# Optimization experiments

Measured on AMD Instinct MI355X. Metric: run time of the kernel, lower is better.

## Reference

```python
import jax, jax.numpy as jnp
import numpy as np

B, N, T, F_IN, H, E_RAND = 4, 1024, 12, 64, 64, 32768


def _xavier_uniform(key, shape):
    fan_in, fan_out = shape[1], shape[0]
    a = np.sqrt(6.0 / (fan_in + fan_out)).astype(np.float32)
    return jax.random.uniform(key, shape, jnp.float32, -a, a)


def setup_inputs() -> dict:
    key = jax.random.key(0)
    ks = jax.random.split(key, 6)
    x = jax.random.normal(ks[0], (B, N, T, F_IN), jnp.float32)
    src = jax.random.randint(ks[1], (E_RAND,), 0, N)
    dst = jax.random.randint(ks[2], (E_RAND,), 0, N)
    loops = jnp.arange(N)  # self-loops: guarantee every softmax row is non-empty
    edge_index = jnp.stack([jnp.concatenate([src, loops]),
                            jnp.concatenate([dst, loops])]).astype(jnp.int64)
    W = _xavier_uniform(ks[3], (H, F_IN))        # nn.Linear weight layout [out, in]
    a_l = _xavier_uniform(ks[4], (H, 1))
    a_r = _xavier_uniform(ks[5], (H, 1))
    bias = jnp.zeros((H,), jnp.float32)
    return {"x": x, "edge_index": edge_index, "W": W, "a_l": a_l, "a_r": a_r, "bias": bias}


def reference(x, edge_index, W, a_l, a_r, bias):
    n = x.shape[1]
    x_in = x.transpose(0, 2, 1, 3)                       # [B,T,N,F_in]
    h = jnp.einsum('btnf,hf->btnh', x_in, W)             # [B,T,N,H]
    attn_l = h @ a_l                                     # [B,T,N,1]
    attn_r = h @ a_r                                     # [B,T,N,1]
    e = attn_l + attn_r.transpose(0, 1, 3, 2)            # [B,T,N,N]
    e = jnp.where(e >= 0, e, 0.2 * e)                    # leaky_relu(0.2)
    adj = jnp.zeros((n, n), dtype=bool).at[edge_index[0], edge_index[1]].set(True)
    e = jnp.where(adj, e, -jnp.inf)                      # mask non-edges
    alpha = jax.nn.softmax(e, axis=-1)                   # row softmax over neighbors
    out = jnp.einsum('btij,btjh->btih', alpha, h) + bias # aggregate
    out = out.transpose(0, 2, 1, 3)                      # back to [B,N,T,H]
    return jax.nn.gelu(out, approximate=False)
```

## Files before the change

### kernel.cpp

```cpp
#include <hip/hip_runtime.h>

#define NNODE 1024
#define TT 12
#define NBT 48
#define CAP 128


__global__ __launch_bounds__(256) void zero_adj(uint4* __restrict__ adj) {
    adj[blockIdx.x * 256 + threadIdx.x] = uint4{0, 0, 0, 0};
}


__global__ __launch_bounds__(256) void scatter_adj(const int* __restrict__ ei, int E,
                                                   unsigned char* __restrict__ adj) {
    int e = blockIdx.x * 256 + threadIdx.x;
    if (e < E) {
        int s = ei[e];
        int d = ei[E + e];
        adj[s * NNODE + d] = 1;
    }
}


__global__ __launch_bounds__(256) void csr_and_h(const unsigned char* __restrict__ adj,
                                                 int* __restrict__ deg,
                                                 int* __restrict__ col,
                                                 const float* __restrict__ x,
                                                 const float* __restrict__ W,
                                                 const float* __restrict__ a_l,
                                                 const float* __restrict__ a_r,
                                                 float* __restrict__ hbuf,
                                                 float* __restrict__ al,
                                                 float* __restrict__ ar) {
    __shared__ float Wt[64 * 65];
    __shared__ float xs[4][8 * 64];
    int tid = threadIdx.x, w = tid >> 6, lane = tid & 63;

    if (blockIdx.x < 256) {
        int i = blockIdx.x * 4 + w;
        const uint4* row = (const uint4*)(adj + (size_t)i * NNODE);
        uint4 v = row[lane];
        unsigned int words[4] = {v.x, v.y, v.z, v.w};
        int cnt = 0;
        #pragma unroll
        for (int q = 0; q < 4; q++) cnt += __popc(words[q] & 0x01010101u);

        int incl = cnt;
        #pragma unroll
        for (int o = 1; o < 64; o <<= 1) {
            int tv = __shfl_up(incl, o);
            if (lane >= o) incl += tv;
        }
        int total = __shfl(incl, 63);
        int excl = incl - cnt;
        if (lane == 0) deg[i] = total;

        int* outp = col + i * CAP + excl;
        int base = lane * 16;
        int idx = 0;
        #pragma unroll
        for (int q = 0; q < 4; q++)
            #pragma unroll
            for (int b = 0; b < 4; b++)
                if ((words[q] >> (8 * b)) & 1) outp[idx++] = base + q * 4 + b;
        return;
    }

    int bidx = blockIdx.x - 256;
    int bt = bidx >> 5;
    int n0 = (bidx & 31) * 32 + w * 8;
    int b = bt / TT, t = bt % TT;

    for (int idx = tid; idx < 4096; idx += 256) {
        int hh = idx >> 6, f = idx & 63;
        Wt[f * 65 + hh] = W[idx];
    }
    const float* xb = x + ((size_t)(b * NNODE + n0) * TT + t) * 64;
    #pragma unroll
    for (int r = 0; r < 8; r++)
        xs[w][r * 64 + lane] = xb[(size_t)r * TT * 64 + lane];
    __syncthreads();

    float acc[8] = {0, 0, 0, 0, 0, 0, 0, 0};
    #pragma unroll 16
    for (int f = 0; f < 64; f++) {
        float wv = Wt[f * 65 + lane];
        #pragma unroll
        for (int r = 0; r < 8; r++)
            acc[r] = fmaf(xs[w][r * 64 + f], wv, acc[r]);
    }

    float alc = a_l[lane], arc = a_r[lane];
    float* hb = hbuf + ((size_t)bt * NNODE + n0) * 64;
    #pragma unroll
    for (int r = 0; r < 8; r++) {
        hb[r * 64 + lane] = acc[r];
        float sl = acc[r] * alc, sr = acc[r] * arc;
        #pragma unroll
        for (int o = 32; o > 0; o >>= 1) {
            sl += __shfl_xor(sl, o);
            sr += __shfl_xor(sr, o);
        }
        if (lane == 0) {
            al[bt * NNODE + n0 + r] = sl;
            ar[bt * NNODE + n0 + r] = sr;
        }
    }
}


__global__ __launch_bounds__(384) void aggregate(const float* __restrict__ hbuf,
                                                 const float* __restrict__ al,
                                                 const float* __restrict__ ar,
                                                 const int* __restrict__ deg,
                                                 const int* __restrict__ col,
                                                 const float* __restrict__ bias,
                                                 float* __restrict__ out) {
    __shared__ int2 pl[6][CAP];
    int w = threadIdx.x >> 6, lane = threadIdx.x & 63;
    int i = blockIdx.x >> 3;
    int g = blockIdx.x & 7;
    int bt = g * 6 + w;
    int b = bt / TT, t = bt % TT;

    int d = deg[i];
    const int* ci = col + i * CAP;
    float ali = al[bt * NNODE + i];
    const float* arb = ar + bt * NNODE;

    int c0 = 0, c1 = 0;
    float e0 = -1e30f, e1 = -1e30f;
    if (lane < d) {
        c0 = ci[lane];
        float e = ali + arb[c0];
        e0 = (e >= 0.f) ? e : 0.2f * e;
    }
    if (lane + 64 < d) {
        c1 = ci[lane + 64];
        float e = ali + arb[c1];
        e1 = (e >= 0.f) ? e : 0.2f * e;
    }
    float m = fmaxf(e0, e1);
    #pragma unroll
    for (int o = 32; o > 0; o >>= 1) m = fmaxf(m, __shfl_xor(m, o));
    float p0 = (lane < d) ? __expf(e0 - m) : 0.f;
    float p1 = (lane + 64 < d) ? __expf(e1 - m) : 0.f;
    float s = p0 + p1;
    #pragma unroll
    for (int o = 32; o > 0; o >>= 1) s += __shfl_xor(s, o);
    if (lane < d) pl[w][lane] = make_int2(c0, __float_as_int(p0));
    if (lane + 64 < d) pl[w][lane + 64] = make_int2(c1, __float_as_int(p1));

    const float* hb = hbuf + (size_t)bt * NNODE * 64;
    float acc = 0.f;
    #pragma unroll 4
    for (int k = 0; k < d; k++) {
        int2 cp = pl[w][k];
        acc = fmaf(__int_as_float(cp.y), hb[cp.x * 64 + lane], acc);
    }
    float v = acc * (1.f / s) + bias[lane];
    float gl = 0.5f * v * (1.f + erff(v * 0.70710678118654752f));
    out[((size_t)(b * NNODE + i) * TT + t) * 64 + lane] = gl;
}


extern "C" void kernel_launch(void* const* d_in, const int* in_sizes, int n_in,
                              void* d_out, int out_size, void* d_ws, size_t ws_size,
                              hipStream_t stream) {
    const float* x    = (const float*)d_in[0];
    const int*   ei   = (const int*)d_in[1];
    const float* W    = (const float*)d_in[2];
    const float* a_l  = (const float*)d_in[3];
    const float* a_r  = (const float*)d_in[4];
    const float* bias = (const float*)d_in[5];
    float* out = (float*)d_out;
    int E = in_sizes[1] / 2;

    char* ws = (char*)d_ws;
    unsigned char* adj = (unsigned char*)ws;
    int* deg = (int*)(ws + (1 << 20));
    int* col = (int*)(ws + (1 << 20) + 8192);
    float* hbuf = (float*)(ws + (2 << 20));
    float* al = (float*)(ws + (2 << 20) + (size_t)NBT * NNODE * 64 * 4);
    float* ar = al + NBT * NNODE;

    zero_adj<<<256, 256, 0, stream>>>((uint4*)adj);
    scatter_adj<<<(E + 255) / 256, 256, 0, stream>>>(ei, E, adj);
    csr_and_h<<<256 + NBT * 32, 256, 0, stream>>>(adj, deg, col, x, W, a_l, a_r, hbuf, al, ar);
    aggregate<<<NNODE * 8, 384, 0, stream>>>(hbuf, al, ar, deg, col, bias, out);
}
```

Baseline: 68.40 us.

## Store h in bf16, use bitmask adjacency, and gather two neighbors per wave

Stores the projected features h as bf16 instead of fp32, halving the traffic of the gather-heavy aggregation. The adjacency is rebuilt as a 1024x32-word bitmask filled with atomicOr, shrinking the zeroing and CSR-building work, and CSR extraction now walks set bits with ffs. The aggregate kernel splits each wave into two halves that process alternating neighbors, each lane loading two bf16 values at once, and then combines the halves with a shuffle. The cost is reduced precision of h in the weighted sum, plus atomics during adjacency construction.

```diff
diff --git a/kernel.cpp b/kernel.cpp
--- a/kernel.cpp
+++ b/kernel.cpp
@@ -4,69 +4,73 @@
 #define TT 12
 #define NBT 48
 #define CAP 128
-
-
-__global__ __launch_bounds__(256) void zero_adj(uint4* __restrict__ adj) {
-    adj[blockIdx.x * 256 + threadIdx.x] = uint4{0, 0, 0, 0};
+#define WORDS 32
+
+__device__ __forceinline__ unsigned short f2bf(float f) {
+    unsigned int u = __float_as_uint(f);
+    u = (u + 0x7fffu + ((u >> 16) & 1u)) >> 16;
+    return (unsigned short)u;
+}
+__device__ __forceinline__ float bf2f(unsigned int v) {
+    return __uint_as_float(v << 16);
+}
+
+
+__global__ __launch_bounds__(256) void zero_bm(uint4* __restrict__ bm) {
+    bm[blockIdx.x * 256 + threadIdx.x] = uint4{0, 0, 0, 0};
 }
 
 
 __global__ __launch_bounds__(256) void scatter_adj(const int* __restrict__ ei, int E,
-                                                   unsigned char* __restrict__ adj) {
+                                                   unsigned int* __restrict__ bm) {
     int e = blockIdx.x * 256 + threadIdx.x;
     if (e < E) {
         int s = ei[e];
         int d = ei[E + e];
-        adj[s * NNODE + d] = 1;
-    }
-}
-
-
-__global__ __launch_bounds__(256) void csr_and_h(const unsigned char* __restrict__ adj,
+        atomicOr(&bm[s * WORDS + (d >> 5)], 1u << (d & 31));
+    }
+}
+
+
+__global__ __launch_bounds__(256) void csr_and_h(const unsigned int* __restrict__ bm,
                                                  int* __restrict__ deg,
                                                  int* __restrict__ col,
                                                  const float* __restrict__ x,
                                                  const float* __restrict__ W,
                                                  const float* __restrict__ a_l,
                                                  const float* __restrict__ a_r,
-                                                 float* __restrict__ hbuf,
+                                                 unsigned short* __restrict__ hbuf,
                                                  float* __restrict__ al,
                                                  float* __restrict__ ar) {
     __shared__ float Wt[64 * 65];
     __shared__ float xs[4][8 * 64];
     int tid = threadIdx.x, w = tid >> 6, lane = tid & 63;
-
-    if (blockIdx.x < 256) {
-        int i = blockIdx.x * 4 + w;
-        const uint4* row = (const uint4*)(adj + (size_t)i * NNODE);
-        uint4 v = row[lane];
-        unsigned int words[4] = {v.x, v.y, v.z, v.w};
-        int cnt = 0;
-        #pragma unroll
-        for (int q = 0; q < 4; q++) cnt += __popc(words[q] & 0x01010101u);
-
+    int half = lane >> 5, sub = lane & 31;
+
+    if (blockIdx.x < 128) {
+        int i = blockIdx.x * 8 + w * 2 + half;
+        unsigned int word = bm[i * WORDS + sub];
+        int cnt = __popc(word);
         int incl = cnt;
         #pragma unroll
-        for (int o = 1; o < 64; o <<= 1) {
-            int tv = __shfl_up(incl, o);
-            if (lane >= o) incl += tv;
-        }
-        int total = __shfl(incl, 63);
+        for (int o = 1; o < 32; o <<= 1) {
+            int tv = __shfl_up(incl, o, 32);
+            if (sub >= o) incl += tv;
+        }
+        int total = __shfl(incl, 31, 32);
         int excl = incl - cnt;
-        if (lane == 0) deg[i] = total;
-
+        if (sub == 0) deg[i] = total;
         int* outp = col + i * CAP + excl;
-        int base = lane * 16;
-        int idx = 0;
-        #pragma unroll
-        for (int q = 0; q < 4; q++)
-            #pragma unroll
-            for (int b = 0; b < 4; b++)
-                if ((words[q] >> (8 * b)) & 1) outp[idx++] = base + q * 4 + b;
+        int idx = 0, base = sub * 32;
+        while (word) {
+            int b = __ffs(word) - 1;
+            word &= word - 1;
+            outp[idx++] = base + b;
+        }
         return;
     }
 
-    int bidx = blockIdx.x - 256;
+    int bidx = blockIdx.x - 128;
     int bt = bidx >> 5;
     int n0 = (bidx & 31) * 32 + w * 8;
     int b = bt / TT, t = bt % TT;
@@ -91,10 +95,10 @@
     }
 
     float alc = a_l[lane], arc = a_r[lane];
-    float* hb = hbuf + ((size_t)bt * NNODE + n0) * 64;
+    unsigned short* hb = hbuf + ((size_t)bt * NNODE + n0) * 64;
     #pragma unroll
     for (int r = 0; r < 8; r++) {
-        hb[r * 64 + lane] = acc[r];
+        hb[r * 64 + lane] = f2bf(acc[r]);
         float sl = acc[r] * alc, sr = acc[r] * arc;
         #pragma unroll
         for (int o = 32; o > 0; o >>= 1) {
@@ -109,7 +113,7 @@
 }
 
 
-__global__ __launch_bounds__(384) void aggregate(const float* __restrict__ hbuf,
+__global__ __launch_bounds__(384) void aggregate(const unsigned short* __restrict__ hbuf,
                                                  const float* __restrict__ al,
                                                  const float* __restrict__ ar,
                                                  const int* __restrict__ deg,
@@ -118,6 +122,7 @@
                                                  float* __restrict__ out) {
     __shared__ int2 pl[6][CAP];
     int w = threadIdx.x >> 6, lane = threadIdx.x & 63;
+    int half = lane >> 5, sub = lane & 31;
     int i = blockIdx.x >> 3;
     int g = blockIdx.x & 7;
     int bt = g * 6 + w;
@@ -151,16 +156,30 @@
     if (lane < d) pl[w][lane] = make_int2(c0, __float_as_int(p0));
     if (lane + 64 < d) pl[w][lane + 64] = make_int2(c1, __float_as_int(p1));
 
-    const float* hb = hbuf + (size_t)bt * NNODE * 64;
-    float acc = 0.f;
-    #pragma unroll 4
-    for (int k = 0; k < d; k++) {
-        int2 cp = pl[w][k];
-        acc = fmaf(__int_as_float(cp.y), hb[cp.x * 64 + lane], acc);
-    }
-    float v = acc * (1.f / s) + bias[lane];
-    float gl = 0.5f * v * (1.f + erff(v * 0.70710678118654752f));
-    out[((size_t)(b * NNODE + i) * TT + t) * 64 + lane] = gl;
+    const unsigned short* hb = hbuf + (size_t)bt * NNODE * 64;
+    float a0 = 0.f, a1 = 0.f;
+    #pragma unroll 8
+    for (int k = 0; k < d; k += 2) {
+        int kk = k + half;
+        int2 cp = (kk < d) ? pl[w][kk] : make_int2(0, 0);
+        unsigned int hv = *(const unsigned int*)(hb + cp.x * 64 + 2 * sub);
+        float pv = __int_as_float(cp.y);
+        a0 = fmaf(pv, bf2f(hv & 0xffffu), a0);
+        a1 = fmaf(pv, bf2f(hv >> 16), a1);
+    }
+    a0 += __shfl_xor(a0, 32);
+    a1 += __shfl_xor(a1, 32);
+
+    float inv = 1.f / s;
+    float2 bb = ((const float2*)bias)[sub];
+    float v0 = a0 * inv + bb.x;
+    float v1 = a1 * inv + bb.y;
+    float g0 = 0.5f * v0 * (1.f + erff(v0 * 0.70710678118654752f));
+    float g1 = 0.5f * v1 * (1.f + erff(v1 * 0.70710678118654752f));
+    if (half == 0) {
+        float2* op = (float2*)(out + ((size_t)(b * NNODE + i) * TT + t) * 64);
+        op[sub] = make_float2(g0, g1);
+    }
 }
 
 
@@ -177,15 +196,15 @@
     int E = in_sizes[1] / 2;
 
     char* ws = (char*)d_ws;
-    unsigned char* adj = (unsigned char*)ws;
-    int* deg = (int*)(ws + (1 << 20));
-    int* col = (int*)(ws + (1 << 20) + 8192);
-    float* hbuf = (float*)(ws + (2 << 20));
-    float* al = (float*)(ws + (2 << 20) + (size_t)NBT * NNODE * 64 * 4);
+    unsigned int* bm = (unsigned int*)ws;
+    int* deg = (int*)(ws + (128 << 10));
+    int* col = (int*)(ws + (128 << 10) + 8192);
+    unsigned short* hbuf = (unsigned short*)(ws + (1 << 20));
+    float* al = (float*)(ws + (1 << 20) + (size_t)NBT * NNODE * 64 * 2);
     float* ar = al + NBT * NNODE;
 
-    zero_adj<<<256, 256, 0, stream>>>((uint4*)adj);
-    scatter_adj<<<(E + 255) / 256, 256, 0, stream>>>(ei, E, adj);
-    csr_and_h<<<256 + NBT * 32, 256, 0, stream>>>(adj, deg, col, x, W, a_l, a_r, hbuf, al, ar);
+    zero_bm<<<32, 256, 0, stream>>>((uint4*)bm);
+    scatter_adj<<<(E + 255) / 256, 256, 0, stream>>>(ei, E, bm);
+    csr_and_h<<<128 + NBT * 32, 256, 0, stream>>>(bm, deg, col, x, W, a_l, a_r, hbuf, al, ar);
     aggregate<<<NNODE * 8, 384, 0, stream>>>(hbuf, al, ar, deg, col, bias, out);
 }
```

Result: faster. 64.61 us (-5.5%).
